# Optimization experiments

Hardware: AMD Instinct MI355X
Metric: run time of the kernel (lower is better)

The kernel has to match this reference:

```python
import jax, jax.numpy as jnp
import numpy as np

N = 4096      # nodes
F = 256       # dim_feat
D = 64        # dim_hid == dim_readout
H = 4         # nheads
ALPHA = 0.2   # LeakyReLU negative slope
NEG = jnp.float32(-9e15)


def setup_inputs() -> dict:
    key = jax.random.key(0)
    ks = jax.random.split(key, 6)
    x = jax.random.normal(ks[0], (N, F), jnp.float32)
    adj = jax.random.randint(ks[1], (N, N), 0, 2, jnp.int32)  # dense 0/1 adjacency
    W1 = jax.random.normal(ks[2], (H, F, D), jnp.float32) * (1.414 / (F ** 0.5))
    a1 = jax.random.normal(ks[3], (H, 2 * D), jnp.float32) * 0.1
    W2 = jax.random.normal(ks[4], (H, H * D, D), jnp.float32) * (1.414 / ((H * D) ** 0.5))
    a2 = jax.random.normal(ks[5], (H, 2 * D), jnp.float32) * 0.1
    t = jnp.zeros((), jnp.float32)
    return {"t": t, "x": x, "adj": adj, "W1": W1, "a1": a1, "W2": W2, "a2": a2}


def _gat_layer(x, adj, W, a):
    """Multi-head dense GAT layer; heads vectorized, outputs concatenated.

    The original builds an [N, N, 2D] concat tensor and multiplies by a [2D,1]
    vector; this factorizes exactly as e_ij = leakyrelu(a1.h_i + a2.h_j).
    """
    h = jnp.einsum('nf,hfd->hnd', x, W)                 # [H,N,D]
    f1 = jnp.einsum('hnd,hd->hn', h, a[:, :D])          # a . h_i part
    f2 = jnp.einsum('hnd,hd->hn', h, a[:, D:])          # a . h_j part
    e = jax.nn.leaky_relu(f1[:, :, None] + f2[:, None, :], ALPHA)  # [H,N,N]
    e = jnp.where(adj[None, :, :] > 0, e, NEG)
    att = jax.nn.softmax(e, axis=-1)                    # row-wise softmax
    out = jax.nn.elu(jnp.einsum('hnm,hmd->hnd', att, h))
    n = x.shape[0]
    return out.transpose(1, 0, 2).reshape(n, -1)        # concat heads -> [N, H*D]


def reference(t, x, adj, W1, a1, W2, a2):
    h1 = _gat_layer(x, adj, W1, a1)   # [N, H*D]
    return _gat_layer(h1, adj, W2, a2)  # [N, H*D]
```

## Files before the change

### kernel.cpp

```cpp
#include <hip/hip_runtime.h>
#include <hip/hip_bf16.h>

#define N_NODES 4096
#define DIMC    256
#define NHEADS  4
#define LOG2E   1.44269504f

typedef __attribute__((ext_vector_type(8))) short  short8;
typedef __attribute__((ext_vector_type(4))) short  short4v;
typedef __attribute__((ext_vector_type(4))) float  float4v;

union S8U { short8 v; unsigned int u[4]; };

#if __has_builtin(__builtin_amdgcn_exp2f)
#define EXP2(x) __builtin_amdgcn_exp2f(x)
#else
#define EXP2(x) exp2f(x)
#endif

__device__ inline unsigned short bf16_bits(__hip_bfloat16 b) {
  union { __hip_bfloat16 b; unsigned short u; } cv; cv.b = b; return cv.u;
}

__device__ inline size_t packidx(int r, int k) {
  return ((size_t)(r >> 4) * 8 + (k >> 5)) * 512
       + (((k >> 3) & 3) * 16 + (r & 15)) * 8 + (k & 7);
}

__global__ __launch_bounds__(256) void prep_kernel(
    const int* __restrict__ adj, unsigned long long* __restrict__ bits,
    const float* __restrict__ x,
    unsigned short* __restrict__ xh, unsigned short* __restrict__ xl,
    const float* __restrict__ W1, const float* __restrict__ W2,
    unsigned short* __restrict__ w1h, unsigned short* __restrict__ w1l,
    unsigned short* __restrict__ w2h, unsigned short* __restrict__ w2l,
    float* __restrict__ f12zero)
{
  int b = blockIdx.x, t = threadIdx.x;
  if (b < 65536) {
    int wid  = b * 4 + (t >> 6);
    int lane = t & 63;
    int row  = wid >> 6;
    int w64  = wid & 63;
    int v = adj[(size_t)row * N_NODES + w64 * 64 + lane];
    unsigned long long m = __ballot(v > 0);
    if (lane == 0) bits[row * 64 + w64] = m;
  } else if (b < 66048) {
    int g = (b - 65536) * 256 + t;
    int n = g >> 5, kb = (g & 31) * 8;
    const float* ip = x + (size_t)n * DIMC + kb;
    float4v v0 = *reinterpret_cast<const float4v*>(ip);
    float4v v1 = *reinterpret_cast<const float4v*>(ip + 4);
    short8 oh, ol;
#pragma unroll
    for (int i = 0; i < 8; ++i) {
      float f = (i < 4) ? v0[i] : v1[i - 4];
      __hip_bfloat16 hb = __float2bfloat16(f);
      oh[i] = (short)bf16_bits(hb);
      ol[i] = (short)bf16_bits(__float2bfloat16(f - __bfloat162float(hb)));
    }
    size_t idx = packidx(n, kb);
    *reinterpret_cast<short8*>(xh + idx) = oh;
    *reinterpret_cast<short8*>(xl + idx) = ol;
  } else if (b < 66112) {
    int bid = b - 66048;
    const float* W = (bid >> 5) ? W2 : W1;
    unsigned short* hi = (bid >> 5) ? w2h : w1h;
    unsigned short* lo = (bid >> 5) ? w2l : w1l;
    int g = (bid & 31) * 256 + t;
    int c = g >> 5, kb = (g & 31) * 8;
    int h = c >> 6, d = c & 63;
    const float* wp = W + (size_t)h * DIMC * 64 + (size_t)kb * 64 + d;
    short8 oh, ol;
#pragma unroll
    for (int i = 0; i < 8; ++i) {
      float f = wp[i * 64];
      __hip_bfloat16 hb = __float2bfloat16(f);
      oh[i] = (short)bf16_bits(hb);
      ol[i] = (short)bf16_bits(__float2bfloat16(f - __bfloat162float(hb)));
    }
    size_t idx = packidx(c, kb);
    *reinterpret_cast<short8*>(hi + idx) = oh;
    *reinterpret_cast<short8*>(lo + idx) = ol;
  } else {
    int z = b - 66112;
    reinterpret_cast<float4v*>(f12zero)[(size_t)z * 256 + t] = {0, 0, 0, 0};
  }
}

__global__ __launch_bounds__(256) void gemm_kernel(
    const unsigned short* __restrict__ Ah, const unsigned short* __restrict__ Al,
    const unsigned short* __restrict__ Bh, const unsigned short* __restrict__ Bl,
    const float* __restrict__ avec,
    float* __restrict__ f1L, float* __restrict__ f2L,
    unsigned short* __restrict__ Bpack)
{
  __shared__ float tl[32][33];
  int t = threadIdx.x;
  int wv = t >> 6, lane = t & 63, quad = lane >> 4, col = lane & 15;
  int bc = blockIdx.y * 32;
  int rt = blockIdx.x * 2 + (wv >> 1);
  int ct = blockIdx.y * 2 + (wv & 1);
  int r0 = blockIdx.x * 32 + (wv >> 1) * 16;
  int c0 = bc + (wv & 1) * 16;
  float4v aHH = {0,0,0,0}, aHL = {0,0,0,0}, aLH = {0,0,0,0};
  const unsigned short* ahp = Ah + (size_t)rt * 4096 + lane * 8;
  const unsigned short* alp = Al + (size_t)rt * 4096 + lane * 8;
  const unsigned short* bhp = Bh + (size_t)ct * 4096 + lane * 8;
  const unsigned short* blp = Bl + (size_t)ct * 4096 + lane * 8;
#pragma unroll
  for (int ks = 0; ks < 8; ++ks) {
    short8 ah = *reinterpret_cast<const short8*>(ahp + ks * 512);
    short8 al = *reinterpret_cast<const short8*>(alp + ks * 512);
    short8 bh = *reinterpret_cast<const short8*>(bhp + ks * 512);
    short8 bl = *reinterpret_cast<const short8*>(blp + ks * 512);
    aHH = __builtin_amdgcn_mfma_f32_16x16x32_bf16(ah, bh, aHH, 0, 0, 0);
    aHL = __builtin_amdgcn_mfma_f32_16x16x32_bf16(ah, bl, aHL, 0, 0, 0);
    aLH = __builtin_amdgcn_mfma_f32_16x16x32_bf16(al, bh, aLH, 0, 0, 0);
  }
  float4v acc = aHH + aHL + aLH;

  int hh = blockIdx.y >> 1;
  int d0 = (c0 + col) & 63;
  float av1 = avec[hh * 128 + d0];
  float av2 = avec[hh * 128 + 64 + d0];
#pragma unroll
  for (int r = 0; r < 4; ++r) {
    float v1 = acc[r] * av1;
    float v2 = acc[r] * av2;
#pragma unroll
    for (int o = 8; o >= 1; o >>= 1) {
      v1 += __shfl_xor(v1, o);
      v2 += __shfl_xor(v2, o);
    }
    if ((lane & 15) == 0) {
      int n = r0 + quad * 4 + r;
      atomicAdd(f1L + hh * N_NODES + n, v1 * LOG2E);
      atomicAdd(f2L + hh * N_NODES + n, v2 * LOG2E);
    }
  }

  int lr = (wv >> 1) * 16 + quad * 4, lc = (wv & 1) * 16 + col;
#pragma unroll
  for (int r = 0; r < 4; ++r) tl[lr + r][lc] = acc[r];
  __syncthreads();
  int tr = t >> 3, tc = (t & 7) * 4;
  short4v oh;
#pragma unroll
  for (int k = 0; k < 4; ++k)
    oh[k] = (short)bf16_bits(__float2bfloat16(tl[tc + k][tr]));
  int c = bc + tr;
  int h = c >> 6, d = c & 63, db = d >> 4, colp = d & 15;
  int quadp = tc >> 3, jj = tc & 7;
  size_t fragu = (((size_t)(h * 128 + blockIdx.x) * 4 + db) * 64
                  + quadp * 16 + colp) * 8 + jj;
  *reinterpret_cast<short4v*>(Bpack + fragu) = oh;
}

__global__ __launch_bounds__(512, 4) void attn_kernel(
    const unsigned short* __restrict__ Bpack,
    const float* __restrict__ f1L, const float* __restrict__ f2L,
    const unsigned long long* __restrict__ bits64,
    float* __restrict__ outf, unsigned short* __restrict__ outhi,
    unsigned short* __restrict__ outlo)
{
  __shared__ __align__(16) float part[8][32][68];
  unsigned long long* lds_bits =
      reinterpret_cast<unsigned long long*>(&part[0][0][0]);
  float* red = reinterpret_cast<float*>(&part[2][0][0]);
  int t = threadIdx.x;
  int wv = t >> 6, lane = t & 63, quad = lane >> 4, col = lane & 15;
  int it = blockIdx.x, h = blockIdx.y;
  int i0 = it * 32;
  int irow0 = i0 + col;
  int irow1 = i0 + 16 + col;

  const float* f2h = f2L + h * N_NODES;
  const unsigned short* bp =
      Bpack + ((size_t)(h * 128 + wv * 16)) * 4 * 512 + lane * 8;
  int jbase = wv * 512;

  short8 b0n = *reinterpret_cast<const short8*>(bp);
  short8 b1n = *reinterpret_cast<const short8*>(bp + 512);
  short8 b2n = *reinterpret_cast<const short8*>(bp + 1024);
  short8 b3n = *reinterpret_cast<const short8*>(bp + 1536);
  float4v fa_n = *reinterpret_cast<const float4v*>(f2h + jbase + quad * 8);
  float4v fb_n = *reinterpret_cast<const float4v*>(f2h + jbase + quad * 8 + 4);

  {
    int rr = t >> 4, tt = (t & 15) * 4;
    const unsigned long long* gsrc = bits64 + (size_t)(i0 + rr) * 64 + tt;
    unsigned long long m0 = gsrc[0], m1 = gsrc[1], m2 = gsrc[2], m3 = gsrc[3];
    lds_bits[(tt + 0) * 32 + rr] = m0;
    lds_bits[(tt + 1) * 32 + rr] = m1;
    lds_bits[(tt + 2) * 32 + rr] = m2;
    lds_bits[(tt + 3) * 32 + rr] = m3;
  }

  {
    float4v ma = *reinterpret_cast<const float4v*>(f2h + t * 8);
    float4v mb = *reinterpret_cast<const float4v*>(f2h + t * 8 + 4);
    red[t] = fmaxf(fmaxf(fmaxf(ma[0], ma[1]), fmaxf(ma[2], ma[3])),
                   fmaxf(fmaxf(mb[0], mb[1]), fmaxf(mb[2], mb[3])));
  }
  __syncthreads();
#pragma unroll
  for (int s2 = 256; s2 >= 1; s2 >>= 1) {
    if (t < s2) red[t] = fmaxf(red[t], red[t + s2]);
    __syncthreads();
  }
  float f2m = red[0];

  float f1i0 = f1L[h * N_NODES + irow0];
  float f1i1 = f1L[h * N_NODES + irow1];
  float s00 = f1i0 + f2m;
  float m0 = fmaxf(s00, 0.2f * s00);
  float f1m0 = f1i0 - m0;
  float cm0 = -0.8f * m0;
  float s01 = f1i1 + f2m;
  float m1 = fmaxf(s01, 0.2f * s01);
  float f1m1 = f1i1 - m1;
  float cm1 = -0.8f * m1;

  float4v acc0[4] = {{0,0,0,0},{0,0,0,0},{0,0,0,0},{0,0,0,0}};
  float4v acc1[4] = {{0,0,0,0},{0,0,0,0},{0,0,0,0},{0,0,0,0}};
  float4v accl0 = {0, 0, 0, 0}, accl1 = {0, 0, 0, 0};
  S8U ones;
  ones.u[0] = ones.u[1] = ones.u[2] = ones.u[3] = 0x3F803F80u;

  for (int s = 0; s < 16; ++s) {
    short8 b0 = b0n, b1 = b1n, b2 = b2n, b3 = b3n;
    float4v fa = fa_n, fb = fb_n;
    if (s < 15) {
      const unsigned short* bs = bp + (size_t)(s + 1) * 2048;
      b0n = *reinterpret_cast<const short8*>(bs);
      b1n = *reinterpret_cast<const short8*>(bs + 512);
      b2n = *reinterpret_cast<const short8*>(bs + 1024);
      b3n = *reinterpret_cast<const short8*>(bs + 1536);
      const float* fp = f2h + jbase + (s + 1) * 32 + quad * 8;
      fa_n = *reinterpret_cast<const float4v*>(fp);
      fb_n = *reinterpret_cast<const float4v*>(fp + 4);
    }
    int j0 = jbase + s * 32;
    int tg = j0 >> 6;
    unsigned long long wq0 = lds_bits[tg * 32 + col];
    unsigned long long wq1 = lds_bits[tg * 32 + col + 16];
    int sh = (j0 & 32) | (quad * 8);
    unsigned wb0 = (unsigned)(wq0 >> sh);
    unsigned wb1 = (unsigned)(wq1 >> sh);
    float w0[8], w1[8];
#pragma unroll
    for (int jj = 0; jj < 8; ++jj) {
      float fv = (jj < 4) ? fa[jj] : fb[jj - 4];
      float sp0 = f1m0 + fv;
      float tb0 = __builtin_fmaf(0.2f, sp0, cm0);
      float e0 = EXP2(fmaxf(sp0, tb0));
      w0[jj] = (wb0 & (1u << jj)) ? e0 : 0.0f;
      float sp1 = f1m1 + fv;
      float tb1 = __builtin_fmaf(0.2f, sp1, cm1);
      float e1 = EXP2(fmaxf(sp1, tb1));
      w1[jj] = (wb1 & (1u << jj)) ? e1 : 0.0f;
    }
    S8U afr0, afr1;
#pragma unroll
    for (int k2 = 0; k2 < 4; ++k2) {
      afr0.u[k2] = __builtin_amdgcn_perm(__float_as_uint(w0[2 * k2 + 1]),
                                         __float_as_uint(w0[2 * k2]),
                                         0x07060302u);
      afr1.u[k2] = __builtin_amdgcn_perm(__float_as_uint(w1[2 * k2 + 1]),
                                         __float_as_uint(w1[2 * k2]),
                                         0x07060302u);
    }
    acc0[0] = __builtin_amdgcn_mfma_f32_16x16x32_bf16(afr0.v, b0, acc0[0], 0, 0, 0);
    acc0[1] = __builtin_amdgcn_mfma_f32_16x16x32_bf16(afr0.v, b1, acc0[1], 0, 0, 0);
    acc0[2] = __builtin_amdgcn_mfma_f32_16x16x32_bf16(afr0.v, b2, acc0[2], 0, 0, 0);
    acc0[3] = __builtin_amdgcn_mfma_f32_16x16x32_bf16(afr0.v, b3, acc0[3], 0, 0, 0);
    accl0   = __builtin_amdgcn_mfma_f32_16x16x32_bf16(afr0.v, ones.v, accl0, 0, 0, 0);
    acc1[0] = __builtin_amdgcn_mfma_f32_16x16x32_bf16(afr1.v, b0, acc1[0], 0, 0, 0);
    acc1[1] = __builtin_amdgcn_mfma_f32_16x16x32_bf16(afr1.v, b1, acc1[1], 0, 0, 0);
    acc1[2] = __builtin_amdgcn_mfma_f32_16x16x32_bf16(afr1.v, b2, acc1[2], 0, 0, 0);
    acc1[3] = __builtin_amdgcn_mfma_f32_16x16x32_bf16(afr1.v, b3, acc1[3], 0, 0, 0);
    accl1   = __builtin_amdgcn_mfma_f32_16x16x32_bf16(afr1.v, ones.v, accl1, 0, 0, 0);
  }

  __syncthreads();

#pragma unroll
  for (int db = 0; db < 4; ++db)
#pragma unroll
    for (int r = 0; r < 4; ++r) {
      part[wv][quad * 4 + r][db * 16 + col] = acc0[db][r];
      part[wv][16 + quad * 4 + r][db * 16 + col] = acc1[db][r];
    }
  if (col == 0) {
#pragma unroll
    for (int r = 0; r < 4; ++r) {
      part[wv][quad * 4 + r][64] = accl0[r];
      part[wv][16 + quad * 4 + r][64] = accl1[r];
    }
  }
  __syncthreads();

  int row = t >> 4, dd = (t & 15) * 4;
  float4v s = {0, 0, 0, 0};
  float l = 0.f;
#pragma unroll
  for (int w2 = 0; w2 < 8; ++w2) {
    float4v pv = *reinterpret_cast<const float4v*>(&part[w2][row][dd]);
    s += pv;
    l += part[w2][row][64];
  }
  float rl = 1.0f / l;
  float o[4];
#pragma unroll
  for (int r = 0; r < 4; ++r) {
    float v = s[r] * rl;
    o[r] = v > 0.f ? v : EXP2(v * LOG2E) - 1.0f;
  }
  int n2 = i0 + row;
  if (outf) {
    size_t oo = (size_t)n2 * DIMC + h * 64 + dd;
    *reinterpret_cast<float4v*>(outf + oo) = {o[0], o[1], o[2], o[3]};
  } else {
    int cg = h * 64 + dd;
    size_t pidx = packidx(n2, cg);
    short4v ohv, olv;
#pragma unroll
    for (int r = 0; r < 4; ++r) {
      __hip_bfloat16 hb = __float2bfloat16(o[r]);
      ohv[r] = (short)bf16_bits(hb);
      olv[r] = (short)bf16_bits(__float2bfloat16(o[r] - __bfloat162float(hb)));
    }
    *reinterpret_cast<short4v*>(outhi + pidx) = ohv;
    *reinterpret_cast<short4v*>(outlo + pidx) = olv;
  }
}

extern "C" void kernel_launch(void* const* d_in, const int* in_sizes, int n_in,
                              void* d_out, int out_size, void* d_ws, size_t ws_size,
                              hipStream_t stream)
{
  const float* x   = (const float*)d_in[1];
  const int*   adj = (const int*)d_in[2];
  const float* W1  = (const float*)d_in[3];
  const float* a1  = (const float*)d_in[4];
  const float* W2  = (const float*)d_in[5];
  const float* a2  = (const float*)d_in[6];

  char* ws = (char*)d_ws;
  size_t off = 0;
  auto alloc = [&](size_t b) { size_t o = off; off = (off + b + 255) & ~255ULL; return o; };
  size_t o_bits = alloc((size_t)N_NODES * 64 * 8);
  size_t o_w1h  = alloc((size_t)DIMC * DIMC * 2);
  size_t o_w1l  = alloc((size_t)DIMC * DIMC * 2);
  size_t o_w2h  = alloc((size_t)DIMC * DIMC * 2);
  size_t o_w2l  = alloc((size_t)DIMC * DIMC * 2);
  size_t o_xh   = alloc((size_t)N_NODES * DIMC * 2);
  size_t o_xl   = alloc((size_t)N_NODES * DIMC * 2);
  size_t o_bp   = alloc((size_t)N_NODES * DIMC * 2);
  size_t o_x2h  = alloc((size_t)N_NODES * DIMC * 2);
  size_t o_x2l  = alloc((size_t)N_NODES * DIMC * 2);
  size_t o_f12  = alloc((size_t)4 * NHEADS * N_NODES * 4);

  unsigned long long* bits = (unsigned long long*)(ws + o_bits);
  unsigned short* w1h = (unsigned short*)(ws + o_w1h);
  unsigned short* w1l = (unsigned short*)(ws + o_w1l);
  unsigned short* w2h = (unsigned short*)(ws + o_w2h);
  unsigned short* w2l = (unsigned short*)(ws + o_w2l);
  unsigned short* xh  = (unsigned short*)(ws + o_xh);
  unsigned short* xl  = (unsigned short*)(ws + o_xl);
  unsigned short* bpk = (unsigned short*)(ws + o_bp);
  unsigned short* x2h = (unsigned short*)(ws + o_x2h);
  unsigned short* x2l = (unsigned short*)(ws + o_x2l);
  float* f12 = (float*)(ws + o_f12);
  float* f1a = f12;
  float* f2a = f12 + NHEADS * N_NODES;
  float* f1b = f12 + 2 * NHEADS * N_NODES;
  float* f2b = f12 + 3 * NHEADS * N_NODES;

  prep_kernel<<<66176, 256, 0, stream>>>(adj, bits, x, xh, xl, W1, W2,
                                         w1h, w1l, w2h, w2l, f12);

  auto layer = [&](const unsigned short* xih, const unsigned short* xil,
                   const unsigned short* wth, const unsigned short* wtl,
                   const float* av, float* f1p, float* f2p, float* outf,
                   unsigned short* oh, unsigned short* ol) {
    gemm_kernel<<<dim3(128, 8), 256, 0, stream>>>(xih, xil, wth, wtl, av,
                                                  f1p, f2p, bpk);
    attn_kernel<<<dim3(128, 4), 512, 0, stream>>>(bpk, f1p, f2p, bits,
                                                  outf, oh, ol);
  };

  layer(xh,  xl,  w1h, w1l, a1, f1a, f2a, nullptr,       x2h, x2l);
  layer(x2h, x2l, w2h, w2l, a2, f1b, f2b, (float*)d_out, nullptr, nullptr);
}
```

Before: 193.3 us.

## Process 64 query rows per attention block to reuse B fragments

The attention kernel now handles 64 rows per block instead of 32, so each loaded B fragment and f2 vector feeds four MFMA row groups instead of two. The grid halves to 64x4 blocks and the launch bounds drop to 2 blocks per CU to make room for the larger accumulator set and doubled LDS buffer. This targets global and L2 traffic for the packed values. In exchange it raises register pressure and leaves only 256 blocks, which may underfill the GPU's 256 CUs and reduce latency hiding.

Result: no change. 193.0 us (-0.1%).

```diff
diff --git a/kernel.cpp b/kernel.cpp
--- a/kernel.cpp
+++ b/kernel.cpp
@@ -157,23 +157,21 @@
   *reinterpret_cast<short4v*>(Bpack + fragu) = oh;
 }
 
-__global__ __launch_bounds__(512, 4) void attn_kernel(
+__global__ __launch_bounds__(512, 2) void attn_kernel(
     const unsigned short* __restrict__ Bpack,
     const float* __restrict__ f1L, const float* __restrict__ f2L,
     const unsigned long long* __restrict__ bits64,
     float* __restrict__ outf, unsigned short* __restrict__ outhi,
     unsigned short* __restrict__ outlo)
 {
-  __shared__ __align__(16) float part[8][32][68];
+  __shared__ __align__(16) float part[8][64][68];
   unsigned long long* lds_bits =
       reinterpret_cast<unsigned long long*>(&part[0][0][0]);
   float* red = reinterpret_cast<float*>(&part[2][0][0]);
   int t = threadIdx.x;
   int wv = t >> 6, lane = t & 63, quad = lane >> 4, col = lane & 15;
   int it = blockIdx.x, h = blockIdx.y;
-  int i0 = it * 32;
-  int irow0 = i0 + col;
-  int irow1 = i0 + 16 + col;
+  int i0 = it * 64;
 
   const float* f2h = f2L + h * N_NODES;
   const unsigned short* bp =
@@ -188,13 +186,10 @@
   float4v fb_n = *reinterpret_cast<const float4v*>(f2h + jbase + quad * 8 + 4);
 
   {
-    int rr = t >> 4, tt = (t & 15) * 4;
+    int rr = t >> 3, tt = (t & 7) * 8;
     const unsigned long long* gsrc = bits64 + (size_t)(i0 + rr) * 64 + tt;
-    unsigned long long m0 = gsrc[0], m1 = gsrc[1], m2 = gsrc[2], m3 = gsrc[3];
-    lds_bits[(tt + 0) * 32 + rr] = m0;
-    lds_bits[(tt + 1) * 32 + rr] = m1;
-    lds_bits[(tt + 2) * 32 + rr] = m2;
-    lds_bits[(tt + 3) * 32 + rr] = m3;
+#pragma unroll
+    for (int i = 0; i < 8; ++i) lds_bits[(tt + i) * 64 + rr] = gsrc[i];
   }
 
   {
@@ -211,20 +206,24 @@
   }
   float f2m = red[0];
 
-  float f1i0 = f1L[h * N_NODES + irow0];
-  float f1i1 = f1L[h * N_NODES + irow1];
-  float s00 = f1i0 + f2m;
-  float m0 = fmaxf(s00, 0.2f * s00);
-  float f1m0 = f1i0 - m0;
-  float cm0 = -0.8f * m0;
-  float s01 = f1i1 + f2m;
-  float m1 = fmaxf(s01, 0.2f * s01);
-  float f1m1 = f1i1 - m1;
-  float cm1 = -0.8f * m1;
-
-  float4v acc0[4] = {{0,0,0,0},{0,0,0,0},{0,0,0,0},{0,0,0,0}};
-  float4v acc1[4] = {{0,0,0,0},{0,0,0,0},{0,0,0,0},{0,0,0,0}};
-  float4v accl0 = {0, 0, 0, 0}, accl1 = {0, 0, 0, 0};
+  float f1m[4], cm[4];
+#pragma unroll
+  for (int r = 0; r < 4; ++r) {
+    float f1i = f1L[h * N_NODES + i0 + r * 16 + col];
+    float s0 = f1i + f2m;
+    float m = fmaxf(s0, 0.2f * s0);
+    f1m[r] = f1i - m;
+    cm[r] = -0.8f * m;
+  }
+
+  float4v acc[4][4];
+  float4v accl[4];
+#pragma unroll
+  for (int r = 0; r < 4; ++r) {
+    accl[r] = (float4v){0, 0, 0, 0};
+#pragma unroll
+    for (int db = 0; db < 4; ++db) acc[r][db] = (float4v){0, 0, 0, 0};
+  }
   S8U ones;
   ones.u[0] = ones.u[1] = ones.u[2] = ones.u[3] = 0x3F803F80u;
 
@@ -243,96 +242,86 @@
     }
     int j0 = jbase + s * 32;
     int tg = j0 >> 6;
-    unsigned long long wq0 = lds_bits[tg * 32 + col];
-    unsigned long long wq1 = lds_bits[tg * 32 + col + 16];
     int sh = (j0 & 32) | (quad * 8);
-    unsigned wb0 = (unsigned)(wq0 >> sh);
-    unsigned wb1 = (unsigned)(wq1 >> sh);
-    float w0[8], w1[8];
-#pragma unroll
-    for (int jj = 0; jj < 8; ++jj) {
-      float fv = (jj < 4) ? fa[jj] : fb[jj - 4];
-      float sp0 = f1m0 + fv;
-      float tb0 = __builtin_fmaf(0.2f, sp0, cm0);
-      float e0 = EXP2(fmaxf(sp0, tb0));
-      w0[jj] = (wb0 & (1u << jj)) ? e0 : 0.0f;
-      float sp1 = f1m1 + fv;
-      float tb1 = __builtin_fmaf(0.2f, sp1, cm1);
-      float e1 = EXP2(fmaxf(sp1, tb1));
-      w1[jj] = (wb1 & (1u << jj)) ? e1 : 0.0f;
-    }
-    S8U afr0, afr1;
-#pragma unroll
-    for (int k2 = 0; k2 < 4; ++k2) {
-      afr0.u[k2] = __builtin_amdgcn_perm(__float_as_uint(w0[2 * k2 + 1]),
-                                         __float_as_uint(w0[2 * k2]),
-                                         0x07060302u);
-      afr1.u[k2] = __builtin_amdgcn_perm(__float_as_uint(w1[2 * k2 + 1]),
-                                         __float_as_uint(w1[2 * k2]),
-                                         0x07060302u);
-    }
-    acc0[0] = __builtin_amdgcn_mfma_f32_16x16x32_bf16(afr0.v, b0, acc0[0], 0, 0, 0);
-    acc0[1] = __builtin_amdgcn_mfma_f32_16x16x32_bf16(afr0.v, b1, acc0[1], 0, 0, 0);
-    acc0[2] = __builtin_amdgcn_mfma_f32_16x16x32_bf16(afr0.v, b2, acc0[2], 0, 0, 0);
-    acc0[3] = __builtin_amdgcn_mfma_f32_16x16x32_bf16(afr0.v, b3, acc0[3], 0, 0, 0);
-    accl0   = __builtin_amdgcn_mfma_f32_16x16x32_bf16(afr0.v, ones.v, accl0, 0, 0, 0);
-    acc1[0] = __builtin_amdgcn_mfma_f32_16x16x32_bf16(afr1.v, b0, acc1[0], 0, 0, 0);
-    acc1[1] = __builtin_amdgcn_mfma_f32_16x16x32_bf16(afr1.v, b1, acc1[1], 0, 0, 0);
-    acc1[2] = __builtin_amdgcn_mfma_f32_16x16x32_bf16(afr1.v, b2, acc1[2], 0, 0, 0);
-    acc1[3] = __builtin_amdgcn_mfma_f32_16x16x32_bf16(afr1.v, b3, acc1[3], 0, 0, 0);
-    accl1   = __builtin_amdgcn_mfma_f32_16x16x32_bf16(afr1.v, ones.v, accl1, 0, 0, 0);
+#pragma unroll
+    for (int r = 0; r < 4; ++r) {
+      unsigned wb = (unsigned)(lds_bits[tg * 64 + r * 16 + col] >> sh);
+      float w[8];
+#pragma unroll
+      for (int jj = 0; jj < 8; ++jj) {
+        float fv = (jj < 4) ? fa[jj] : fb[jj - 4];
+        float sp = f1m[r] + fv;
+        float tb = __builtin_fmaf(0.2f, sp, cm[r]);
+        float e = EXP2(fmaxf(sp, tb));
+        w[jj] = (wb & (1u << jj)) ? e : 0.0f;
+      }
+      S8U afr;
+#pragma unroll
+      for (int k2 = 0; k2 < 4; ++k2)
+        afr.u[k2] = __builtin_amdgcn_perm(__float_as_uint(w[2 * k2 + 1]),
+                                          __float_as_uint(w[2 * k2]),
+                                          0x07060302u);
+      acc[r][0] = __builtin_amdgcn_mfma_f32_16x16x32_bf16(afr.v, b0, acc[r][0], 0, 0, 0);
+      acc[r][1] = __builtin_amdgcn_mfma_f32_16x16x32_bf16(afr.v, b1, acc[r][1], 0, 0, 0);
+      acc[r][2] = __builtin_amdgcn_mfma_f32_16x16x32_bf16(afr.v, b2, acc[r][2], 0, 0, 0);
+      acc[r][3] = __builtin_amdgcn_mfma_f32_16x16x32_bf16(afr.v, b3, acc[r][3], 0, 0, 0);
+      accl[r]   = __builtin_amdgcn_mfma_f32_16x16x32_bf16(afr.v, ones.v, accl[r], 0, 0, 0);
+    }
   }
 
   __syncthreads();
 
 #pragma unroll
-  for (int db = 0; db < 4; ++db)
-#pragma unroll
-    for (int r = 0; r < 4; ++r) {
-      part[wv][quad * 4 + r][db * 16 + col] = acc0[db][r];
-      part[wv][16 + quad * 4 + r][db * 16 + col] = acc1[db][r];
-    }
-  if (col == 0) {
-#pragma unroll
-    for (int r = 0; r < 4; ++r) {
-      part[wv][quad * 4 + r][64] = accl0[r];
-      part[wv][16 + quad * 4 + r][64] = accl1[r];
+  for (int r = 0; r < 4; ++r) {
+#pragma unroll
+    for (int db = 0; db < 4; ++db)
+#pragma unroll
+      for (int rg = 0; rg < 4; ++rg)
+        part[wv][r * 16 + quad * 4 + rg][db * 16 + col] = acc[r][db][rg];
+    if (col == 0) {
+#pragma unroll
+      for (int rg = 0; rg < 4; ++rg)
+        part[wv][r * 16 + quad * 4 + rg][64] = accl[r][rg];
     }
   }
   __syncthreads();
 
-  int row = t >> 4, dd = (t & 15) * 4;
-  float4v s = {0, 0, 0, 0};
-  float l = 0.f;
-#pragma unroll
-  for (int w2 = 0; w2 < 8; ++w2) {
-    float4v pv = *reinterpret_cast<const float4v*>(&part[w2][row][dd]);
-    s += pv;
-    l += part[w2][row][64];
-  }
-  float rl = 1.0f / l;
-  float o[4];
-#pragma unroll
-  for (int r = 0; r < 4; ++r) {
-    float v = s[r] * rl;
-    o[r] = v > 0.f ? v : EXP2(v * LOG2E) - 1.0f;
-  }
-  int n2 = i0 + row;
-  if (outf) {
-    size_t oo = (size_t)n2 * DIMC + h * 64 + dd;
-    *reinterpret_cast<float4v*>(outf + oo) = {o[0], o[1], o[2], o[3]};
-  } else {
-    int cg = h * 64 + dd;
-    size_t pidx = packidx(n2, cg);
-    short4v ohv, olv;
-#pragma unroll
-    for (int r = 0; r < 4; ++r) {
-      __hip_bfloat16 hb = __float2bfloat16(o[r]);
-      ohv[r] = (short)bf16_bits(hb);
-      olv[r] = (short)bf16_bits(__float2bfloat16(o[r] - __bfloat162float(hb)));
-    }
-    *reinterpret_cast<short4v*>(outhi + pidx) = ohv;
-    *reinterpret_cast<short4v*>(outlo + pidx) = olv;
+#pragma unroll
+  for (int ii = 0; ii < 2; ++ii) {
+    int item = ii * 512 + t;
+    int row = item >> 4, dd = (item & 15) * 4;
+    float4v s = {0, 0, 0, 0};
+    float l = 0.f;
+#pragma unroll
+    for (int w2 = 0; w2 < 8; ++w2) {
+      float4v pv = *reinterpret_cast<const float4v*>(&part[w2][row][dd]);
+      s += pv;
+      l += part[w2][row][64];
+    }
+    float rl = 1.0f / l;
+    float o[4];
+#pragma unroll
+    for (int rg = 0; rg < 4; ++rg) {
+      float v = s[rg] * rl;
+      o[rg] = v > 0.f ? v : EXP2(v * LOG2E) - 1.0f;
+    }
+    int n2 = i0 + row;
+    if (outf) {
+      size_t oo = (size_t)n2 * DIMC + h * 64 + dd;
+      *reinterpret_cast<float4v*>(outf + oo) = {o[0], o[1], o[2], o[3]};
+    } else {
+      int cg = h * 64 + dd;
+      size_t pidx = packidx(n2, cg);
+      short4v ohv, olv;
+#pragma unroll
+      for (int rg = 0; rg < 4; ++rg) {
+        __hip_bfloat16 hb = __float2bfloat16(o[rg]);
+        ohv[rg] = (short)bf16_bits(hb);
+        olv[rg] = (short)bf16_bits(__float2bfloat16(o[rg] - __bfloat162float(hb)));
+      }
+      *reinterpret_cast<short4v*>(outhi + pidx) = ohv;
+      *reinterpret_cast<short4v*>(outlo + pidx) = olv;
+    }
   }
 }
 
@@ -387,8 +376,8 @@
                    unsigned short* oh, unsigned short* ol) {
     gemm_kernel<<<dim3(128, 8), 256, 0, stream>>>(xih, xil, wth, wtl, av,
                                                   f1p, f2p, bpk);
-    attn_kernel<<<dim3(128, 4), 512, 0, stream>>>(bpk, f1p, f2p, bits,
-                                                  outf, oh, ol);
+    attn_kernel<<<dim3(64, 4), 512, 0, stream>>>(bpk, f1p, f2p, bits,
+                                                 outf, oh, ol);
   };
 
   layer(xh,  xl,  w1h, w1l, a1, f1a, f2a, nullptr,       x2h, x2l);
```
